# Kernel optimization log

Hardware: AMD Instinct MI355X
Metric: run time of the kernel (lower is better)

Reference implementation:

```python
import jax, jax.numpy as jnp
import numpy as np

N_QUBITS = 8
N_LAYERS = 1
DIM = 1 << N_QUBITS  # 256 statevector amplitudes; PennyLane wire 0 = most significant bit

_idx = np.arange(DIM)
_BITS = np.stack([(_idx >> (N_QUBITS - 1 - w)) & 1 for w in range(N_QUBITS)])  # (n, D)
_FLIP = np.stack([_idx ^ (1 << (N_QUBITS - 1 - w)) for w in range(N_QUBITS)])  # (n, D)

def _cnot_perm(c, t):
    return _idx ^ (((_idx >> (N_QUBITS - 1 - c)) & 1) << (N_QUBITS - 1 - t))

_CNOT_NP = [_cnot_perm(w, w + 1) for w in range(N_QUBITS - 1)] + [_cnot_perm(N_QUBITS - 1, 0)]
BITS = jnp.asarray(_BITS)
FLIP = jnp.asarray(_FLIP)
CNOTS = [jnp.asarray(p) for p in _CNOT_NP]


def _ry(t):
    c = jnp.cos(t / 2)
    s = jnp.sin(t / 2)
    return jnp.stack([jnp.stack([c, -s], -1), jnp.stack([s, c], -1)], -2).astype(jnp.complex64)


def _rx(t):
    c = jnp.cos(t / 2).astype(jnp.complex64)
    s = (-1j) * jnp.sin(t / 2).astype(jnp.complex64)
    return jnp.stack([jnp.stack([c, s], -1), jnp.stack([s, c], -1)], -2)


def _rz(t):
    tc = t.astype(jnp.complex64)
    e0 = jnp.exp(-0.5j * tc)
    e1 = jnp.exp(0.5j * tc)
    z = jnp.zeros_like(e0)
    return jnp.stack([jnp.stack([e0, z], -1), jnp.stack([z, e1], -1)], -2)


def _apply(state, U, w):
    # state: (B, 2**n) complex64; U: (2,2) shared or (B,2,2) per-sample; wire w (MSB-first)
    B = state.shape[0]
    s = state.reshape(B, 1 << w, 2, -1)
    if U.ndim == 3:
        s = jnp.einsum('bij,bajc->baic', U, s)
    else:
        s = jnp.einsum('ij,bajc->baic', U, s)
    return s.reshape(B, DIM)


def _circuit(angles, weights):
    # angles: (B, n_qubits) float32; weights: (n_layers, n_qubits, 3) float32
    B = angles.shape[0]
    state = jnp.zeros((B, DIM), jnp.complex64).at[:, 0].set(1.0)
    for w in range(N_QUBITS):
        state = _apply(state, _ry(angles[:, w]), w)  # per-sample RY encoding
    for l in range(N_LAYERS):
        for w in range(N_QUBITS):
            state = _apply(state, _rx(weights[l, w, 0]), w)
            state = _apply(state, _ry(weights[l, w, 1]), w)
            state = _apply(state, _rz(weights[l, w, 2]), w)
        for p in CNOTS:  # CNOT ring entangler as basis permutation
            state = state[:, p]
    probs = jnp.abs(state) ** 2
    outs = []
    for w in range(N_QUBITS):
        overlap = jnp.conj(state) * state[:, FLIP[w]]
        sign = (1.0 - 2.0 * BITS[w]).astype(probs.dtype)
        outs.append(jnp.sum(jnp.real(overlap), -1))       # <X_w>
        outs.append(jnp.sum(sign * jnp.imag(overlap), -1))  # <Y_w>
        outs.append(jnp.sum(sign * probs, -1))            # <Z_w>
    return jnp.stack(outs, -1)  # (B, 3*n_qubits), order X0,Y0,Z0,X1,...


def setup_inputs() -> dict:
    key = jax.random.key(0)
    k1, k2, k3 = jax.random.split(key, 3)
    B, IN_DIM = 16384, 512
    h = jax.random.normal(k1, (B, IN_DIM), jnp.float32)
    W_pre = 0.02 * jax.random.normal(k2, (N_QUBITS, IN_DIM), jnp.float32)
    b_pre = jnp.zeros((N_QUBITS,), jnp.float32)
    weights = 0.01 * jax.random.normal(k3, (N_LAYERS, N_QUBITS, 3), jnp.float32)
    return {"h": h, "W_pre": W_pre, "b_pre": b_pre, "weights": weights}


def reference(h, W_pre, b_pre, weights):
    a = h @ W_pre.T + b_pre
    a = jnp.clip(jnp.tanh(a) * (jnp.pi / 2), -jnp.pi, jnp.pi)  # _scale_to_angles
    z = _circuit(a, weights)
    norm = jnp.linalg.norm(z, axis=-1, keepdims=True)
    return z / jnp.maximum(norm, 1e-12)  # F.normalize(dim=-1)
```

## Files before the change

### kernel.cpp

```cpp
#include <hip/hip_runtime.h>


__global__ __launch_bounds__(256) void vqc_gemv(
    const float* __restrict__ h,
    const float* __restrict__ Wp,
    float* __restrict__ aw,
    int B)
{
    const int lane = threadIdx.x & 63;
    const int wave = (blockIdx.x * blockDim.x + threadIdx.x) >> 6;
    const int nwv  = (gridDim.x * blockDim.x) >> 6;

    const float4* W4 = (const float4*)Wp;
    float wf[8][8];
    #pragma unroll
    for (int q = 0; q < 8; ++q) {
        float4 v0 = W4[q * 128 + lane * 2 + 0];
        float4 v1 = W4[q * 128 + lane * 2 + 1];
        wf[q][0] = v0.x; wf[q][1] = v0.y; wf[q][2] = v0.z; wf[q][3] = v0.w;
        wf[q][4] = v1.x; wf[q][5] = v1.y; wf[q][6] = v1.z; wf[q][7] = v1.w;
    }

    const int b3 = (lane >> 3) & 1, b4 = (lane >> 4) & 1, b5 = (lane >> 5) & 1;
    const float4* H4 = (const float4*)h;

    const int row0 = wave * 2;
    if (row0 >= B) return;

    float4 h00 = H4[row0 * 128 + lane * 2 + 0];
    float4 h01 = H4[row0 * 128 + lane * 2 + 1];
    int row1 = row0 + 1;
    float4 h10 = H4[(row1 < B ? row1 : row0) * 128 + lane * 2 + 0];
    float4 h11 = H4[(row1 < B ? row1 : row0) * 128 + lane * 2 + 1];

    float hf0[8] = { h00.x, h00.y, h00.z, h00.w, h01.x, h01.y, h01.z, h01.w };
    float hf1[8] = { h10.x, h10.y, h10.z, h10.w, h11.x, h11.y, h11.z, h11.w };

    float acc0[8], acc1[8];
    #pragma unroll
    for (int q = 0; q < 8; ++q) {
        float a0 = 0.f, a1 = 0.f;
        #pragma unroll
        for (int j = 0; j < 8; ++j) {
            a0 = fmaf(wf[q][j], hf0[j], a0);
            a1 = fmaf(wf[q][j], hf1[j], a1);
        }
        acc0[q] = a0; acc1[q] = a1;
    }

    float n0[4], n1[4];
    #pragma unroll
    for (int j = 0; j < 4; ++j) {
        float k0 = b3 ? acc0[1 + 2*j] : acc0[0 + 2*j];
        float s0 = b3 ? acc0[0 + 2*j] : acc0[1 + 2*j];
        float k1 = b3 ? acc1[1 + 2*j] : acc1[0 + 2*j];
        float s1 = b3 ? acc1[0 + 2*j] : acc1[1 + 2*j];
        n0[j] = k0 + __shfl_xor(s0, 8);
        n1[j] = k1 + __shfl_xor(s1, 8);
    }
    float m0[2], m1[2];
    #pragma unroll
    for (int i = 0; i < 2; ++i) {
        float k0 = b4 ? n0[1 + 2*i] : n0[0 + 2*i];
        float s0 = b4 ? n0[0 + 2*i] : n0[1 + 2*i];
        float k1 = b4 ? n1[1 + 2*i] : n1[0 + 2*i];
        float s1 = b4 ? n1[0 + 2*i] : n1[1 + 2*i];
        m0[i] = k0 + __shfl_xor(s0, 16);
        m1[i] = k1 + __shfl_xor(s1, 16);
    }
    float v0, v1;
    {
        float k0 = b5 ? m0[1] : m0[0];
        float s0 = b5 ? m0[0] : m0[1];
        float k1 = b5 ? m1[1] : m1[0];
        float s1 = b5 ? m1[0] : m1[1];
        v0 = k0 + __shfl_xor(s0, 32);
        v1 = k1 + __shfl_xor(s1, 32);
    }
    v0 += __shfl_xor(v0, 1); v1 += __shfl_xor(v1, 1);
    v0 += __shfl_xor(v0, 2); v1 += __shfl_xor(v1, 2);
    v0 += __shfl_xor(v0, 4); v1 += __shfl_xor(v1, 4);

    if ((lane & 7) == 0) {
        int q = lane >> 3;
        aw[row0 * 8 + q] = v0;
        if (row1 < B) aw[row1 * 8 + q] = v1;
    }
}

__global__ __launch_bounds__(256) void vqc_epilogue(
    const float* __restrict__ aw,
    const float* __restrict__ bp,
    const float* __restrict__ wt,
    float* __restrict__ out,
    int B)
{
    const int row = blockIdx.x * blockDim.x + threadIdx.x;
    if (row >= B) return;

    const float4* A4 = (const float4*)aw;
    float4 a0 = A4[row * 2 + 0];
    float4 a1 = A4[row * 2 + 1];
    float av[8] = { a0.x, a0.y, a0.z, a0.w, a1.x, a1.y, a1.z, a1.w };

    float X[8], Y[8], Z[8];
    #pragma unroll
    for (int q = 0; q < 8; ++q) {
        float t0 = wt[q * 3 + 0] * 0.5f;
        float t1 = wt[q * 3 + 1] * 0.5f;
        float t2 = wt[q * 3 + 2] * 0.5f;
        float s0, c0, s1, c1, sz, cz;
        __sincosf(t0, &s0, &c0);
        __sincosf(t1, &s1, &c1);
        __sincosf(t2, &sz, &cz);
        float N00r =  c1 * c0, N00i =  s1 * s0;
        float N01r = -s1 * c0, N01i = -c1 * s0;
        float N10r =  s1 * c0, N10i = -c1 * s0;
        float N11r =  c1 * c0, N11i = -s1 * s0;
        float M00r = cz * N00r + sz * N00i, M00i = cz * N00i - sz * N00r;
        float M01r = cz * N01r + sz * N01i, M01i = cz * N01i - sz * N01r;
        float M10r = cz * N10r - sz * N10i, M10i = cz * N10i + sz * N10r;
        float M11r = cz * N11r - sz * N11i, M11i = cz * N11i + sz * N11r;

        float a = av[q] + bp[q];
        a = fminf(fmaxf(a, -15.f), 15.f);
        float e = __expf(a + a);
        float th = (e - 1.f) / (e + 1.f);
        float phi = th * 0.78539816339744831f;
        float ss, cc;
        __sincosf(phi, &ss, &cc);
        float ar = M00r * cc + M01r * ss, ai = M00i * cc + M01i * ss;
        float br = M10r * cc + M11r * ss, bi = M10i * cc + M11i * ss;
        Z[q] = (ar * ar + ai * ai) - (br * br + bi * bi);
        X[q] = 2.f * (ar * br + ai * bi);
        Y[q] = 2.f * (ar * bi - ai * br);
    }

    float P[8], T[8];
    P[0] = Z[0];
    #pragma unroll
    for (int w = 1; w < 8; ++w) P[w] = P[w - 1] * Z[w];
    T[7] = Z[7];
    #pragma unroll
    for (int w = 6; w >= 0; --w) T[w] = Z[w] * T[w + 1];
    float Z2to6 = Z[2] * Z[3] * Z[4] * Z[5] * Z[6];

    float o[24];
    #pragma unroll
    for (int w = 0; w < 7; ++w) o[3 * w] = X[w] * X[w + 1];
    o[21] = X[7] * X[0] * X[1];
    o[1] = X[0] * Y[1] * T[2];
    #pragma unroll
    for (int w = 1; w < 7; ++w) o[3 * w + 1] = Y[w] * X[w + 1] * P[w - 1];
    o[22] = -Y[7] * Y[0] * Y[1] * Z2to6;
    o[2] = T[1];
    #pragma unroll
    for (int w = 1; w < 8; ++w) o[3 * w + 2] = P[w];

    float sq = 0.f;
    #pragma unroll
    for (int j = 0; j < 24; ++j) sq = fmaf(o[j], o[j], sq);
    float inv = 1.f / fmaxf(sqrtf(sq), 1e-12f);

    float4* O4 = (float4*)(out + row * 24);
    #pragma unroll
    for (int j = 0; j < 6; ++j) {
        float4 vv = { o[4 * j] * inv, o[4 * j + 1] * inv,
                      o[4 * j + 2] * inv, o[4 * j + 3] * inv };
        O4[j] = vv;
    }
}

extern "C" void kernel_launch(void* const* d_in, const int* in_sizes, int n_in,
                              void* d_out, int out_size, void* d_ws, size_t ws_size,
                              hipStream_t stream) {
    const float* h  = (const float*)d_in[0];
    const float* Wp = (const float*)d_in[1];
    const float* bp = (const float*)d_in[2];
    const float* wt = (const float*)d_in[3];
    float* out = (float*)d_out;
    float* aw  = (float*)d_ws;

    const int B = in_sizes[0] / 512;
    const int nblk1 = (B + 511) / 512;
    vqc_gemv<<<nblk1 * 128, 256, 0, stream>>>(h, Wp, aw, B);
    vqc_epilogue<<<(B + 255) / 256, 256, 0, stream>>>(aw, bp, wt, out, B);
}
```

Before: 83.45 us.

## Fuse GEMV and circuit epilogue into one kernel with 8 rows per wave

Merges the projection GEMV and the analytic circuit epilogue into a single kernel. Each wave now processes 8 rows, issuing all 16 float4 loads up front, and hands the 8 angle values per row to 8 lanes through shuffles. Those lanes then evaluate the epilogue and write the outputs. This removes the second launch and the workspace round-trip, and gives more loads in flight per wave. In exchange only 8 of 64 lanes run the epilogue, there are 4x fewer waves, and register pressure rises, and there is no bounds check on row0+r for the loads.

```diff
diff --git a/kernel.cpp b/kernel.cpp
--- a/kernel.cpp
+++ b/kernel.cpp
@@ -1,15 +1,18 @@
 #include <hip/hip_runtime.h>
 
 
-__global__ __launch_bounds__(256) void vqc_gemv(
+__global__ __launch_bounds__(256) void vqc_fused(
     const float* __restrict__ h,
     const float* __restrict__ Wp,
-    float* __restrict__ aw,
+    const float* __restrict__ bp,
+    const float* __restrict__ wt,
+    float* __restrict__ out,
     int B)
 {
     const int lane = threadIdx.x & 63;
     const int wave = (blockIdx.x * blockDim.x + threadIdx.x) >> 6;
-    const int nwv  = (gridDim.x * blockDim.x) >> 6;
+    const int row0 = wave * 8;
+    if (row0 >= B) return;
 
     const float4* W4 = (const float4*)Wp;
     float wf[8][8];
@@ -21,153 +24,129 @@
         wf[q][4] = v1.x; wf[q][5] = v1.y; wf[q][6] = v1.z; wf[q][7] = v1.w;
     }
 
-    const int b3 = (lane >> 3) & 1, b4 = (lane >> 4) & 1, b5 = (lane >> 5) & 1;
     const float4* H4 = (const float4*)h;
-
-    const int row0 = wave * 2;
-    if (row0 >= B) return;
-
-    float4 h00 = H4[row0 * 128 + lane * 2 + 0];
-    float4 h01 = H4[row0 * 128 + lane * 2 + 1];
-    int row1 = row0 + 1;
-    float4 h10 = H4[(row1 < B ? row1 : row0) * 128 + lane * 2 + 0];
-    float4 h11 = H4[(row1 < B ? row1 : row0) * 128 + lane * 2 + 1];
-
-    float hf0[8] = { h00.x, h00.y, h00.z, h00.w, h01.x, h01.y, h01.z, h01.w };
-    float hf1[8] = { h10.x, h10.y, h10.z, h10.w, h11.x, h11.y, h11.z, h11.w };
-
-    float acc0[8], acc1[8];
+    float4 ha[8], hb[8];
     #pragma unroll
-    for (int q = 0; q < 8; ++q) {
-        float a0 = 0.f, a1 = 0.f;
-        #pragma unroll
-        for (int j = 0; j < 8; ++j) {
-            a0 = fmaf(wf[q][j], hf0[j], a0);
-            a1 = fmaf(wf[q][j], hf1[j], a1);
-        }
-        acc0[q] = a0; acc1[q] = a1;
+    for (int r = 0; r < 8; ++r) {
+        ha[r] = H4[(row0 + r) * 128 + lane * 2 + 0];
+        hb[r] = H4[(row0 + r) * 128 + lane * 2 + 1];
     }
 
-    float n0[4], n1[4];
+    const int b3 = (lane >> 3) & 1, b4 = (lane >> 4) & 1, b5 = (lane >> 5) & 1;
+
+    float v[8];
     #pragma unroll
-    for (int j = 0; j < 4; ++j) {
-        float k0 = b3 ? acc0[1 + 2*j] : acc0[0 + 2*j];
-        float s0 = b3 ? acc0[0 + 2*j] : acc0[1 + 2*j];
-        float k1 = b3 ? acc1[1 + 2*j] : acc1[0 + 2*j];
-        float s1 = b3 ? acc1[0 + 2*j] : acc1[1 + 2*j];
-        n0[j] = k0 + __shfl_xor(s0, 8);
-        n1[j] = k1 + __shfl_xor(s1, 8);
-    }
-    float m0[2], m1[2];
-    #pragma unroll
-    for (int i = 0; i < 2; ++i) {
-        float k0 = b4 ? n0[1 + 2*i] : n0[0 + 2*i];
-        float s0 = b4 ? n0[0 + 2*i] : n0[1 + 2*i];
-        float k1 = b4 ? n1[1 + 2*i] : n1[0 + 2*i];
-        float s1 = b4 ? n1[0 + 2*i] : n1[1 + 2*i];
-        m0[i] = k0 + __shfl_xor(s0, 16);
-        m1[i] = k1 + __shfl_xor(s1, 16);
-    }
-    float v0, v1;
-    {
-        float k0 = b5 ? m0[1] : m0[0];
-        float s0 = b5 ? m0[0] : m0[1];
-        float k1 = b5 ? m1[1] : m1[0];
-        float s1 = b5 ? m1[0] : m1[1];
-        v0 = k0 + __shfl_xor(s0, 32);
-        v1 = k1 + __shfl_xor(s1, 32);
-    }
-    v0 += __shfl_xor(v0, 1); v1 += __shfl_xor(v1, 1);
-    v0 += __shfl_xor(v0, 2); v1 += __shfl_xor(v1, 2);
-    v0 += __shfl_xor(v0, 4); v1 += __shfl_xor(v1, 4);
-
-    if ((lane & 7) == 0) {
-        int q = lane >> 3;
-        aw[row0 * 8 + q] = v0;
-        if (row1 < B) aw[row1 * 8 + q] = v1;
-    }
-}
-
-__global__ __launch_bounds__(256) void vqc_epilogue(
-    const float* __restrict__ aw,
-    const float* __restrict__ bp,
-    const float* __restrict__ wt,
-    float* __restrict__ out,
-    int B)
-{
-    const int row = blockIdx.x * blockDim.x + threadIdx.x;
-    if (row >= B) return;
-
-    const float4* A4 = (const float4*)aw;
-    float4 a0 = A4[row * 2 + 0];
-    float4 a1 = A4[row * 2 + 1];
-    float av[8] = { a0.x, a0.y, a0.z, a0.w, a1.x, a1.y, a1.z, a1.w };
-
-    float X[8], Y[8], Z[8];
-    #pragma unroll
-    for (int q = 0; q < 8; ++q) {
-        float t0 = wt[q * 3 + 0] * 0.5f;
-        float t1 = wt[q * 3 + 1] * 0.5f;
-        float t2 = wt[q * 3 + 2] * 0.5f;
-        float s0, c0, s1, c1, sz, cz;
-        __sincosf(t0, &s0, &c0);
-        __sincosf(t1, &s1, &c1);
-        __sincosf(t2, &sz, &cz);
-        float N00r =  c1 * c0, N00i =  s1 * s0;
-        float N01r = -s1 * c0, N01i = -c1 * s0;
-        float N10r =  s1 * c0, N10i = -c1 * s0;
-        float N11r =  c1 * c0, N11i = -s1 * s0;
-        float M00r = cz * N00r + sz * N00i, M00i = cz * N00i - sz * N00r;
-        float M01r = cz * N01r + sz * N01i, M01i = cz * N01i - sz * N01r;
-        float M10r = cz * N10r - sz * N10i, M10i = cz * N10i + sz * N10r;
-        float M11r = cz * N11r - sz * N11i, M11i = cz * N11i + sz * N11r;
-
-        float a = av[q] + bp[q];
-        a = fminf(fmaxf(a, -15.f), 15.f);
-        float e = __expf(a + a);
-        float th = (e - 1.f) / (e + 1.f);
-        float phi = th * 0.78539816339744831f;
-        float ss, cc;
-        __sincosf(phi, &ss, &cc);
-        float ar = M00r * cc + M01r * ss, ai = M00i * cc + M01i * ss;
-        float br = M10r * cc + M11r * ss, bi = M10i * cc + M11i * ss;
-        Z[q] = (ar * ar + ai * ai) - (br * br + bi * bi);
-        X[q] = 2.f * (ar * br + ai * bi);
-        Y[q] = 2.f * (ar * bi - ai * br);
+    for (int r = 0; r < 8; ++r) {
+        float hf[8] = { ha[r].x, ha[r].y, ha[r].z, ha[r].w,
+                        hb[r].x, hb[r].y, hb[r].z, hb[r].w };
+        float acc[8];
+        #pragma unroll
+        for (int q = 0; q < 8; ++q) {
+            float a = 0.f;
+            #pragma unroll
+            for (int j = 0; j < 8; ++j) a = fmaf(wf[q][j], hf[j], a);
+            acc[q] = a;
+        }
+        float n[4];
+        #pragma unroll
+        for (int j = 0; j < 4; ++j) {
+            float k = b3 ? acc[1 + 2 * j] : acc[0 + 2 * j];
+            float s = b3 ? acc[0 + 2 * j] : acc[1 + 2 * j];
+            n[j] = k + __shfl_xor(s, 8);
+        }
+        float m[2];
+        #pragma unroll
+        for (int i = 0; i < 2; ++i) {
+            float k = b4 ? n[1 + 2 * i] : n[0 + 2 * i];
+            float s = b4 ? n[0 + 2 * i] : n[1 + 2 * i];
+            m[i] = k + __shfl_xor(s, 16);
+        }
+        float k = b5 ? m[1] : m[0];
+        float s = b5 ? m[0] : m[1];
+        float vv = k + __shfl_xor(s, 32);
+        vv += __shfl_xor(vv, 1);
+        vv += __shfl_xor(vv, 2);
+        vv += __shfl_xor(vv, 4);
+        v[r] = vv;
     }
 
-    float P[8], T[8];
-    P[0] = Z[0];
+    float t = v[0];
     #pragma unroll
-    for (int w = 1; w < 8; ++w) P[w] = P[w - 1] * Z[w];
-    T[7] = Z[7];
+    for (int k2 = 1; k2 < 8; ++k2) t = ((lane & 7) == k2) ? v[k2] : t;
+
+    float av[8];
     #pragma unroll
-    for (int w = 6; w >= 0; --w) T[w] = Z[w] * T[w + 1];
-    float Z2to6 = Z[2] * Z[3] * Z[4] * Z[5] * Z[6];
+    for (int q = 0; q < 8; ++q) av[q] = __shfl(t, q * 8 + (lane & 7));
 
-    float o[24];
-    #pragma unroll
-    for (int w = 0; w < 7; ++w) o[3 * w] = X[w] * X[w + 1];
-    o[21] = X[7] * X[0] * X[1];
-    o[1] = X[0] * Y[1] * T[2];
-    #pragma unroll
-    for (int w = 1; w < 7; ++w) o[3 * w + 1] = Y[w] * X[w + 1] * P[w - 1];
-    o[22] = -Y[7] * Y[0] * Y[1] * Z2to6;
-    o[2] = T[1];
-    #pragma unroll
-    for (int w = 1; w < 8; ++w) o[3 * w + 2] = P[w];
+    if (lane < 8 && row0 + lane < B) {
+        const int row = row0 + lane;
 
-    float sq = 0.f;
-    #pragma unroll
-    for (int j = 0; j < 24; ++j) sq = fmaf(o[j], o[j], sq);
-    float inv = 1.f / fmaxf(sqrtf(sq), 1e-12f);
+        float X[8], Y[8], Z[8];
+        #pragma unroll
+        for (int q = 0; q < 8; ++q) {
+            float t0 = wt[q * 3 + 0] * 0.5f;
+            float t1 = wt[q * 3 + 1] * 0.5f;
+            float t2 = wt[q * 3 + 2] * 0.5f;
+            float s0, c0, s1, c1, sz, cz;
+            __sincosf(t0, &s0, &c0);
+            __sincosf(t1, &s1, &c1);
+            __sincosf(t2, &sz, &cz);
+            float N00r =  c1 * c0, N00i =  s1 * s0;
+            float N01r = -s1 * c0, N01i = -c1 * s0;
+            float N10r =  s1 * c0, N10i = -c1 * s0;
+            float N11r =  c1 * c0, N11i = -s1 * s0;
+            float M00r = cz * N00r + sz * N00i, M00i = cz * N00i - sz * N00r;
+            float M01r = cz * N01r + sz * N01i, M01i = cz * N01i - sz * N01r;
+            float M10r = cz * N10r - sz * N10i, M10i = cz * N10i + sz * N10r;
+            float M11r = cz * N11r - sz * N11i, M11i = cz * N11i + sz * N11r;
 
-    float4* O4 = (float4*)(out + row * 24);
-    #pragma unroll
-    for (int j = 0; j < 6; ++j) {
-        float4 vv = { o[4 * j] * inv, o[4 * j + 1] * inv,
-                      o[4 * j + 2] * inv, o[4 * j + 3] * inv };
-        O4[j] = vv;
+            float a = av[q] + bp[q];
+            a = fminf(fmaxf(a, -15.f), 15.f);
+            float e = __expf(a + a);
+            float th = (e - 1.f) / (e + 1.f);
+            float phi = th * 0.78539816339744831f;
+            float ss, cc;
+            __sincosf(phi, &ss, &cc);
+            float ar = M00r * cc + M01r * ss, ai = M00i * cc + M01i * ss;
+            float br = M10r * cc + M11r * ss, bi = M10i * cc + M11i * ss;
+            Z[q] = (ar * ar + ai * ai) - (br * br + bi * bi);
+            X[q] = 2.f * (ar * br + ai * bi);
+            Y[q] = 2.f * (ar * bi - ai * br);
+        }
+
+        float P[8], T[8];
+        P[0] = Z[0];
+        #pragma unroll
+        for (int w = 1; w < 8; ++w) P[w] = P[w - 1] * Z[w];
+        T[7] = Z[7];
+        #pragma unroll
+        for (int w = 6; w >= 0; --w) T[w] = Z[w] * T[w + 1];
+        float Z2to6 = Z[2] * Z[3] * Z[4] * Z[5] * Z[6];
+
+        float o[24];
+        #pragma unroll
+        for (int w = 0; w < 7; ++w) o[3 * w] = X[w] * X[w + 1];
+        o[21] = X[7] * X[0] * X[1];
+        o[1] = X[0] * Y[1] * T[2];
+        #pragma unroll
+        for (int w = 1; w < 7; ++w) o[3 * w + 1] = Y[w] * X[w + 1] * P[w - 1];
+        o[22] = -Y[7] * Y[0] * Y[1] * Z2to6;
+        o[2] = T[1];
+        #pragma unroll
+        for (int w = 1; w < 8; ++w) o[3 * w + 2] = P[w];
+
+        float sq = 0.f;
+        #pragma unroll
+        for (int j = 0; j < 24; ++j) sq = fmaf(o[j], o[j], sq);
+        float inv = 1.f / fmaxf(sqrtf(sq), 1e-12f);
+
+        float4* O4 = (float4*)(out + row * 24);
+        #pragma unroll
+        for (int j = 0; j < 6; ++j) {
+            float4 vv = { o[4 * j] * inv, o[4 * j + 1] * inv,
+                          o[4 * j + 2] * inv, o[4 * j + 3] * inv };
+            O4[j] = vv;
+        }
     }
 }
 
@@ -179,10 +158,9 @@
     const float* bp = (const float*)d_in[2];
     const float* wt = (const float*)d_in[3];
     float* out = (float*)d_out;
-    float* aw  = (float*)d_ws;
 
     const int B = in_sizes[0] / 512;
-    const int nblk1 = (B + 511) / 512;
-    vqc_gemv<<<nblk1 * 128, 256, 0, stream>>>(h, Wp, aw, B);
-    vqc_epilogue<<<(B + 255) / 256, 256, 0, stream>>>(aw, bp, wt, out, B);
+    const int waves = (B + 7) / 8;
+    const int nblk = (waves + 3) / 4;
+    vqc_fused<<<nblk, 256, 0, stream>>>(h, Wp, bp, wt, out, B);
 }
```

After: 87.38 us. 4.7% more time.
